# Optimization experiments

Hardware: AMD Instinct MI355X
Metric: run time of the kernel (lower is better)

The kernel has to match this reference:

```python
import jax, jax.numpy as jnp
import numpy as np

# 47 skeleton edges (parent, child) from getSkeletalModelStructure()
EDGES = np.array([
    (0, 1), (1, 2), (2, 3), (3, 29), (1, 5), (5, 6), (6, 8), (8, 9), (8, 13),
    (8, 17), (8, 21), (8, 25), (9, 10), (10, 11), (11, 12), (13, 14), (14, 15),
    (15, 16), (17, 18), (18, 19), (19, 20), (21, 22), (22, 23), (23, 24),
    (25, 26), (26, 27), (27, 28), (29, 30), (29, 34), (29, 38), (29, 42),
    (29, 46), (30, 31), (31, 32), (32, 33), (34, 35), (35, 36), (36, 37),
    (38, 39), (39, 40), (40, 41), (42, 43), (43, 44), (44, 45), (46, 47),
    (47, 48), (48, 49)], dtype=np.int32)

N_JOINTS = 50
N_EDGES = 47


def _length_direct(pose):
    # pose: [B, T, 151]; drop counter channel, view as joints
    B, T = pose.shape[0], pose.shape[1]
    p = pose[..., :-1].reshape(B, T, N_JOINTS, 3)
    diff = p[:, :, EDGES[:, 0], :] - p[:, :, EDGES[:, 1], :]   # [B, T, 47, 3]
    length = jnp.linalg.norm(diff, axis=-1)                      # [B, T, 47]
    eps = jnp.finfo(pose.dtype).tiny
    direct = diff / (length + eps)[..., None]                    # [B, T, 47, 3]
    # torch stacks each [B,T,3] edge dir along dim=-1 -> [B,T,3,47], then reshapes
    directs = jnp.transpose(direct, (0, 1, 3, 2)).reshape(B, T, N_EDGES * 3)
    return length, directs


def setup_inputs() -> dict:
    key = jax.random.key(0)
    k1, k2 = jax.random.split(key)
    B, T, D = 128, 1024, 151
    preds = jax.random.normal(k1, (B, T, D), dtype=jnp.float32)
    targets = jax.random.normal(k2, (B, T, D), dtype=jnp.float32)
    return {"preds": preds, "targets": targets}


def reference(preds, targets):
    target_pad = 0.0
    mask = (targets != target_pad).astype(preds.dtype)           # [B, T, 151]
    preds_m = preds * mask
    targets_m = targets * mask
    _, preds_dir = _length_direct(preds_m)
    _, targets_dir = _length_direct(targets_m)
    preds_dir = preds_dir * mask[:, :, :N_EDGES * 3]
    targets_dir = targets_dir * mask[:, :, :N_EDGES * 3]
    # cfg: loss='l1' (mean abs), vel_loss='mse' (mean square), loss_scale=1.0
    l1 = jnp.mean(jnp.abs(preds_m - targets_m))
    vel_mse = jnp.mean(jnp.square(preds_dir - targets_dir))
    return l1 + 0.1 * vel_mse
```

## Files before the change

### kernel.cpp

```cpp
#include <hip/hip_runtime.h>


#define N_ROWS   (128 * 1024)
#define ROW      151
#define N_EDGES  47
#define GRID     2048
#define BLOCK    256
#define CHUNKS   4
#define CHUNK_ROWS 4
#define CHUNK_DW (CHUNK_ROWS * ROW)
#define CHUNK_TASKS (CHUNK_ROWS * N_EDGES)
#define BUF_DW (2 * CHUNK_DW)

#if __has_builtin(__builtin_amdgcn_rsqf)
__device__ __forceinline__ float fast_rsq(float x) { return __builtin_amdgcn_rsqf(x); }
#else
__device__ __forceinline__ float fast_rsq(float x) {
    float r; asm volatile("v_rsq_f32 %0, %1" : "=v"(r) : "v"(x)); return r;
}
#endif

template <int N>
__device__ __forceinline__ void wait_vm() {
    asm volatile("s_waitcnt vmcnt(%0)" :: "n"(N) : "memory");
}
__device__ __forceinline__ void wait_lgkm0() {
    asm volatile("s_waitcnt lgkmcnt(0)" ::: "memory");
}

__device__ __forceinline__ void dma16(const float* g, float* l) {
    __builtin_amdgcn_global_load_lds(
        (const __attribute__((address_space(1))) unsigned*)g,
        (__attribute__((address_space(3))) unsigned*)l, 16, 0, 0);
}

__device__ __forceinline__ void dma_chunk(const float* gp, const float* gt,
                                          float* L, int lane) {
    const int l4 = lane * 4;
    dma16(gp + l4,        L);
    dma16(gp + 256 + l4,  L + 256);
    dma16(gt + l4,        L + CHUNK_DW);
    dma16(gt + 256 + l4,  L + CHUNK_DW + 256);
    if (lane < 23) {
        dma16(gp + 512 + l4, L + 512);
        dma16(gt + 512 + l4, L + CHUNK_DW + 512);
    }
}

#define E(p, c) ((unsigned)((p) * 3) | ((unsigned)((c) * 3) << 16))
__constant__ unsigned c_edge[N_EDGES] = {
    E(0,1),  E(1,2),  E(2,3),  E(3,29), E(1,5),  E(5,6),  E(6,8),  E(8,9),
    E(8,13), E(8,17), E(8,21), E(8,25), E(9,10), E(10,11),E(11,12),E(13,14),
    E(14,15),E(15,16),E(17,18),E(18,19),E(19,20),E(21,22),E(22,23),E(23,24),
    E(25,26),E(26,27),E(27,28),E(29,30),E(29,34),E(29,38),E(29,42),E(29,46),
    E(30,31),E(31,32),E(32,33),E(34,35),E(35,36),E(36,37),E(38,39),E(39,40),
    E(40,41),E(42,43),E(43,44),E(44,45),E(46,47),E(47,48),E(48,49)};

struct TaskDesc { int act[3], roff[3], pi[3], ci[3], me[3]; };

__device__ __forceinline__ void compute_chunk(
        const float* __restrict__ B, int lane, const TaskDesc& td,
        float& l1, float& vel) {
    const float* __restrict__ Bp = B;
    const float* __restrict__ Bt = B + CHUNK_DW;

#pragma unroll
    for (int k = 0; k < 3; ++k) {
        int i = lane + k * 64;
        if (i < CHUNK_DW / 4) {
            float4 pv = ((const float4*)Bp)[i];
            float4 tv = ((const float4*)Bt)[i];
            float a0 = (tv.x != 0.f) ? pv.x : 0.f;
            float a1 = (tv.y != 0.f) ? pv.y : 0.f;
            float a2 = (tv.z != 0.f) ? pv.z : 0.f;
            float a3 = (tv.w != 0.f) ? pv.w : 0.f;
            l1 += fabsf(a0 - tv.x) + fabsf(a1 - tv.y)
                + fabsf(a2 - tv.z) + fabsf(a3 - tv.w);
        }
    }

#pragma unroll
    for (int k = 0; k < 3; ++k) {
        if (td.act[k]) {
            const float* __restrict__ Rp = Bp + td.roff[k];
            const float* __restrict__ Rt = Bt + td.roff[k];
            int pi = td.pi[k], ci = td.ci[k], me = td.me[k];
            float tpx = Rt[pi], tpy = Rt[pi + 1], tpz = Rt[pi + 2];
            float tcx = Rt[ci], tcy = Rt[ci + 1], tcz = Rt[ci + 2];
            float ppx = Rp[pi], ppy = Rp[pi + 1], ppz = Rp[pi + 2];
            float pcx = Rp[ci], pcy = Rp[ci + 1], pcz = Rp[ci + 2];
            float apx = (tpx != 0.f) ? ppx : 0.f;
            float apy = (tpy != 0.f) ? ppy : 0.f;
            float apz = (tpz != 0.f) ? ppz : 0.f;
            float acx = (tcx != 0.f) ? pcx : 0.f;
            float acy = (tcy != 0.f) ? pcy : 0.f;
            float acz = (tcz != 0.f) ? pcz : 0.f;
            float pdx = apx - acx, pdy = apy - acy, pdz = apz - acz;
            float tdx = tpx - tcx, tdy = tpy - tcy, tdz = tpz - tcz;
            float pd2 = pdx * pdx + pdy * pdy + pdz * pdz;
            float td2 = tdx * tdx + tdy * tdy + tdz * tdz;
            float pinv = (pd2 > 0.f) ? fast_rsq(pd2) : 0.f;
            float tinv = (td2 > 0.f) ? fast_rsq(td2) : 0.f;
            float dx = pdx * pinv - tdx * tinv;
            float dy = pdy * pinv - tdy * tinv;
            float dz = pdz * pinv - tdz * tinv;
            float m0 = (Rt[me]      != 0.f) ? 1.f : 0.f;
            float m1 = (Rt[me + 47] != 0.f) ? 1.f : 0.f;
            float m2 = (Rt[me + 94] != 0.f) ? 1.f : 0.f;
            vel += m0 * dx * dx + m1 * dy * dy + m2 * dz * dz;
        }
    }
}

__global__ __launch_bounds__(BLOCK, 8) void reg_loss_main(
        const float* __restrict__ preds, const float* __restrict__ targets,
        float* __restrict__ wsL, float* __restrict__ wsV) {
    __shared__ float S[4][BUF_DW];
    __shared__ float redL[4], redV[4];

    const int t = threadIdx.x;
    const int lane = t & 63;
    const int wave = t >> 6;
    float* B = &S[wave][0];

    const long long wb =
        (long long)(blockIdx.x * 4 + wave) * (CHUNKS * CHUNK_DW);
    const float* gp = preds + wb;
    const float* gt = targets + wb;

    TaskDesc td;
#pragma unroll
    for (int k = 0; k < 3; ++k) {
        int task = lane + k * 64;
        td.act[k] = task < CHUNK_TASKS;
        int r = task / N_EDGES;
        int e = task - r * N_EDGES;
        if (!td.act[k]) { r = 0; e = 0; }
        td.roff[k] = r * ROW;
        unsigned pk = c_edge[e];
        td.pi[k] = pk & 0xffff;
        td.ci[k] = pk >> 16;
        td.me[k] = e;
    }

    dma_chunk(gp, gt, B, lane);

    float l1 = 0.f, vel = 0.f;

#pragma unroll
    for (int c = 0; c < CHUNKS; ++c) {
        wait_vm<0>();
        compute_chunk(B, lane, td, l1, vel);
        if (c + 1 < CHUNKS) {
            wait_lgkm0();
            dma_chunk(gp + (c + 1) * CHUNK_DW, gt + (c + 1) * CHUNK_DW,
                      B, lane);
        }
    }

#pragma unroll
    for (int off = 32; off > 0; off >>= 1) {
        l1  += __shfl_down(l1, off);
        vel += __shfl_down(vel, off);
    }
    if (lane == 0) { redL[wave] = l1; redV[wave] = vel; }
    __syncthreads();
    if (t == 0) {
        wsL[blockIdx.x] = redL[0] + redL[1] + redL[2] + redL[3];
        wsV[blockIdx.x] = redV[0] + redV[1] + redV[2] + redV[3];
    }
}

__global__ __launch_bounds__(BLOCK) void reg_loss_finalize(
        const float* __restrict__ wsL, const float* __restrict__ wsV,
        float* __restrict__ out) {
    __shared__ double rl[4], rv[4];
    const int t = threadIdx.x;
    const int lane = t & 63;
    const int wave = t >> 6;
    double L = 0.0, V = 0.0;
    for (int k = t; k < GRID; k += BLOCK) { L += wsL[k]; V += wsV[k]; }
#pragma unroll
    for (int off = 32; off > 0; off >>= 1) {
        L += __shfl_down(L, off);
        V += __shfl_down(V, off);
    }
    if (lane == 0) { rl[wave] = L; rv[wave] = V; }
    __syncthreads();
    if (t == 0) {
        double Ls = rl[0] + rl[1] + rl[2] + rl[3];
        double Vs = rv[0] + rv[1] + rv[2] + rv[3];
        out[0] = (float)(Ls / ((double)N_ROWS * 151.0)
                       + 0.1 * (Vs / ((double)N_ROWS * 141.0)));
    }
}

extern "C" void kernel_launch(void* const* d_in, const int* in_sizes, int n_in,
                              void* d_out, int out_size, void* d_ws, size_t ws_size,
                              hipStream_t stream) {
    const float* preds   = (const float*)d_in[0];
    const float* targets = (const float*)d_in[1];
    float* wsL = (float*)d_ws;
    float* wsV = wsL + GRID;
    float* out = (float*)d_out;

    reg_loss_main<<<GRID, BLOCK, 0, stream>>>(preds, targets, wsL, wsV);
    reg_loss_finalize<<<1, BLOCK, 0, stream>>>(wsL, wsV, out);
}
```

Baseline: 178.7 us.

## Replace global-to-LDS DMA with register prefetch overlapping edge compute

Chunks are now loaded into registers with float4 global loads instead of global_load_lds transfers. The L1 term is computed directly from those registers, and the values are stored to LDS only for the edge-direction pass. The next chunk's loads are issued before the current chunk's edge computation, so global latency can overlap compute; before, each chunk's load was issued only after the previous compute finished. The cost is extra VGPRs for the prefetch buffers and explicit LDS stores, which may reduce occupancy.

```diff
diff --git a/kernel.cpp b/kernel.cpp
--- a/kernel.cpp
+++ b/kernel.cpp
@@ -20,31 +20,11 @@
 }
 #endif
 
-template <int N>
-__device__ __forceinline__ void wait_vm() {
-    asm volatile("s_waitcnt vmcnt(%0)" :: "n"(N) : "memory");
-}
-__device__ __forceinline__ void wait_lgkm0() {
-    asm volatile("s_waitcnt lgkmcnt(0)" ::: "memory");
-}
-
-__device__ __forceinline__ void dma16(const float* g, float* l) {
-    __builtin_amdgcn_global_load_lds(
-        (const __attribute__((address_space(1))) unsigned*)g,
-        (__attribute__((address_space(3))) unsigned*)l, 16, 0, 0);
-}
-
-__device__ __forceinline__ void dma_chunk(const float* gp, const float* gt,
-                                          float* L, int lane) {
-    const int l4 = lane * 4;
-    dma16(gp + l4,        L);
-    dma16(gp + 256 + l4,  L + 256);
-    dma16(gt + l4,        L + CHUNK_DW);
-    dma16(gt + 256 + l4,  L + CHUNK_DW + 256);
-    if (lane < 23) {
-        dma16(gp + 512 + l4, L + 512);
-        dma16(gt + 512 + l4, L + CHUNK_DW + 512);
-    }
+__device__ __forceinline__ float4 ldg4(const float* __restrict__ p) {
+    return *reinterpret_cast<const float4*>(p);
+}
+__device__ __forceinline__ void st4(float* __restrict__ p, float4 v) {
+    *reinterpret_cast<float4*>(p) = v;
 }
 
 #define E(p, c) ((unsigned)((p) * 3) | ((unsigned)((c) * 3) << 16))
@@ -58,27 +38,19 @@
 
 struct TaskDesc { int act[3], roff[3], pi[3], ci[3], me[3]; };
 
-__device__ __forceinline__ void compute_chunk(
-        const float* __restrict__ B, int lane, const TaskDesc& td,
-        float& l1, float& vel) {
+__device__ __forceinline__ void acc_l1(float4 pv, float4 tv, float& l1) {
+    float a0 = (tv.x != 0.f) ? pv.x : 0.f;
+    float a1 = (tv.y != 0.f) ? pv.y : 0.f;
+    float a2 = (tv.z != 0.f) ? pv.z : 0.f;
+    float a3 = (tv.w != 0.f) ? pv.w : 0.f;
+    l1 += fabsf(a0 - tv.x) + fabsf(a1 - tv.y)
+        + fabsf(a2 - tv.z) + fabsf(a3 - tv.w);
+}
+
+__device__ __forceinline__ void compute_edges(
+        const float* __restrict__ B, const TaskDesc& td, float& vel) {
     const float* __restrict__ Bp = B;
     const float* __restrict__ Bt = B + CHUNK_DW;
-
-#pragma unroll
-    for (int k = 0; k < 3; ++k) {
-        int i = lane + k * 64;
-        if (i < CHUNK_DW / 4) {
-            float4 pv = ((const float4*)Bp)[i];
-            float4 tv = ((const float4*)Bt)[i];
-            float a0 = (tv.x != 0.f) ? pv.x : 0.f;
-            float a1 = (tv.y != 0.f) ? pv.y : 0.f;
-            float a2 = (tv.z != 0.f) ? pv.z : 0.f;
-            float a3 = (tv.w != 0.f) ? pv.w : 0.f;
-            l1 += fabsf(a0 - tv.x) + fabsf(a1 - tv.y)
-                + fabsf(a2 - tv.z) + fabsf(a3 - tv.w);
-        }
-    }
-
 #pragma unroll
     for (int k = 0; k < 3; ++k) {
         if (td.act[k]) {
@@ -128,6 +100,9 @@
     const float* gp = preds + wb;
     const float* gt = targets + wb;
 
+    const int l4 = lane * 4;
+    const bool tail = lane < 23;
+
     TaskDesc td;
 #pragma unroll
     for (int k = 0; k < 3; ++k) {
@@ -143,19 +118,37 @@
         td.me[k] = e;
     }
 
-    dma_chunk(gp, gt, B, lane);
-
     float l1 = 0.f, vel = 0.f;
+    float4 p0, p1, p2, t0, t1, t2;
+
+    p0 = ldg4(gp + l4);       p1 = ldg4(gp + 256 + l4);
+    t0 = ldg4(gt + l4);       t1 = ldg4(gt + 256 + l4);
+    if (tail) { p2 = ldg4(gp + 512 + l4); t2 = ldg4(gt + 512 + l4); }
 
 #pragma unroll
     for (int c = 0; c < CHUNKS; ++c) {
-        wait_vm<0>();
-        compute_chunk(B, lane, td, l1, vel);
+        st4(B + l4,                 p0);
+        st4(B + 256 + l4,           p1);
+        st4(B + CHUNK_DW + l4,      t0);
+        st4(B + CHUNK_DW + 256 + l4, t1);
+        if (tail) {
+            st4(B + 512 + l4,            p2);
+            st4(B + CHUNK_DW + 512 + l4, t2);
+        }
+
+        acc_l1(p0, t0, l1);
+        acc_l1(p1, t1, l1);
+        if (tail) acc_l1(p2, t2, l1);
+
         if (c + 1 < CHUNKS) {
-            wait_lgkm0();
-            dma_chunk(gp + (c + 1) * CHUNK_DW, gt + (c + 1) * CHUNK_DW,
-                      B, lane);
+            const float* cp = gp + (c + 1) * CHUNK_DW;
+            const float* ct = gt + (c + 1) * CHUNK_DW;
+            p0 = ldg4(cp + l4);       p1 = ldg4(cp + 256 + l4);
+            t0 = ldg4(ct + l4);       t1 = ldg4(ct + 256 + l4);
+            if (tail) { p2 = ldg4(cp + 512 + l4); t2 = ldg4(ct + 512 + l4); }
         }
+
+        compute_edges(B, td, vel);
     }
 
 #pragma unroll
```

Result: slower. 195.0 us (+9.1%).
